# Performance work log

Hardware: AMD Instinct MI355X
Metric: run time of the kernel (lower is better)

The kernel has to match this reference:

```python
import jax, jax.numpy as jnp
import numpy as np


def setup_inputs() -> dict:
    key = jax.random.key(0)
    k1, k2 = jax.random.split(key)
    N, K, D = 32768, 1024, 512
    x = jax.random.normal(k1, (N, D), dtype=jnp.float32)
    centers = jax.random.normal(k2, (K, D), dtype=jnp.float32)
    return {"x": x, "centers": centers}


def reference(x, centers):
    # broadcasted (x[:,None]-c[None])**2 sum without the O(N*K*D) intermediate)
    x_sq = jnp.sum(x * x, axis=-1, keepdims=True)           # [N, 1]
    c_sq = jnp.sum(centers * centers, axis=-1)              # [K]
    cross = jnp.einsum('nd,kd->nk', x, centers)             # [N, K]
    norm_squared = x_sq + c_sq[None, :] - 2.0 * cross       # [N, K]
    # exp(-d/2) / sum_k exp(-d/2) == softmax(-d/2) over clusters
    probabilities = jax.nn.softmax(-0.5 * norm_squared, axis=1)
    return probabilities
```

## Files before the change

kernel.cpp:

```cpp
#include <hip/hip_runtime.h>
#include <stdint.h>


namespace {
constexpr int N_ROWS  = 32768;
constexpr int K_CL    = 1024;
constexpr int D_DIM   = 512;
constexpr int BM      = 64;
constexpr int THREADS = 512;
constexpr int WAVES   = 8;
constexpr int NSLICE  = 16;
}

typedef _Float16 f16_t;
typedef _Float16 f16x8 __attribute__((ext_vector_type(8)));
typedef _Float16 f16x4 __attribute__((ext_vector_type(4)));
typedef float    f32x16 __attribute__((ext_vector_type(16)));
typedef float    f32x4v __attribute__((ext_vector_type(4)));

__global__ __launch_bounds__(64) void prep_kernel(const float* __restrict__ centers,
                                                  f16_t* __restrict__ bpack,
                                                  float* __restrict__ bias) {
  const int col = blockIdx.x, lane = threadIdx.x;
  const int t  = lane >> 2;
  const int ks = (lane >> 1) & 1;
  const int kh = lane & 1;
  const float* src = centers + (size_t)col * D_DIM + lane * 8;
  f16x8 hi;
  float ssq = 0.f;
  #pragma unroll
  for (int i = 0; i < 8; ++i) {
    float v = src[i];
    ssq += v * v;
    hi[i] = (f16_t)v;
  }
  const int jh = col >> 9, cb = (col & 511) >> 5, c32 = col & 31;
  const size_t off = ((size_t)ks * 16 + cb) * 512 + (c32 * 2 + kh) * 8;
  *(f16x8*)(bpack + (size_t)(2 * t + jh) * 16384 + off) = hi;
  for (int o = 32; o; o >>= 1) ssq += __shfl_down(ssq, o, 64);
  if (lane == 0) bias[col] = -0.5f * ssq;
}

__global__ __launch_bounds__(THREADS, 2) void cluster_kernel(
    const float* __restrict__ x, const f16_t* __restrict__ bpack,
    const float* __restrict__ bias, float* __restrict__ out) {
  __shared__ __align__(16) char Ax[64 * 1024];
  __shared__ float red[WAVES * BM];
  __shared__ float fin[BM];

  const int tid  = threadIdx.x;
  const int wid  = tid >> 6;
  const int lane = tid & 63;
  const int l31  = lane & 31;
  const int h    = lane >> 5;
  const int brow = blockIdx.x * BM;

  const char* bbase = (const char*)bpack + wid * 2048 + (l31 * 2 + h) * 16;

#define LOADB8(S, DST)                                                         \
  {                                                                            \
    const char* p_ = bbase + (size_t)((S) & 31) * 32768;                       \
    (DST)[0] = *(const f16x8*)(p_);                       \
    (DST)[1] = *(const f16x8*)(p_ + 1024);                \
    (DST)[2] = *(const f16x8*)(p_ + 16384);               \
    (DST)[3] = *(const f16x8*)(p_ + 17408);               \
    (DST)[4] = *(const f16x8*)(p_ + 32768);               \
    (DST)[5] = *(const f16x8*)(p_ + 33792);               \
    (DST)[6] = *(const f16x8*)(p_ + 49152);               \
    (DST)[7] = *(const f16x8*)(p_ + 50176);               \
  }
#define COMPUTE16(B)                                                           \
  {                                                                            \
    _Pragma("unroll")                                                          \
    for (int j2_ = 0; j2_ < 2; ++j2_)                                          \
      _Pragma("unroll")                                                        \
      for (int ks_ = 0; ks_ < 2; ++ks_)                                        \
        _Pragma("unroll")                                                      \
        for (int c2_ = 0; c2_ < 2; ++c2_)                                      \
          _Pragma("unroll")                                                    \
          for (int rb_ = 0; rb_ < 2; ++rb_)                                    \
            acc[rb_][j2_ * 2 + c2_] = __builtin_amdgcn_mfma_f32_32x32x16_f16(  \
                a[rb_][ks_], (B)[j2_ * 4 + ks_ * 2 + c2_],                     \
                acc[rb_][j2_ * 2 + c2_], 0, 0, 0);                             \
  }

  f16x8 bA[8], bB[8];

  LOADB8(0, bA)

  {
    const float* xsrc = x + (size_t)brow * D_DIM;
    #pragma unroll
    for (int it = 0; it < 16; ++it) {
      const int idx = it * 512 + tid;
      const int r = idx >> 7, f = idx & 127;
      f32x4v v = __builtin_nontemporal_load(
          (const f32x4v*)(xsrc + (size_t)r * D_DIM + f * 4));
      f16x4 h4;
      h4[0] = (f16_t)v[0]; h4[1] = (f16_t)v[1];
      h4[2] = (f16_t)v[2]; h4[3] = (f16_t)v[3];
      *(f16x4*)(Ax + r * 1024 + ((f * 8) ^ ((r & 7) << 4))) = h4;
    }
  }
  __syncthreads();

  f32x16 acc[2][4];
  #pragma unroll
  for (int rb = 0; rb < 2; ++rb)
    #pragma unroll
    for (int cc = 0; cc < 4; ++cc)
      #pragma unroll
      for (int e = 0; e < 16; ++e) acc[rb][cc][e] = 0.f;

  const char* abase0 = Ax + l31 * 1024;
  const int swz = (l31 & 7) << 4;
  const int h16 = h * 16;
  f16x8 a[2][2];

  #pragma unroll
  for (int tt = 0; tt < 8; ++tt) {
    {
      const int T = 2 * tt;
      LOADB8(2 * (T + 1), bB)
      const int o0 = (T * 64 + h16) ^ swz;
      const int o1 = o0 ^ 32;
      a[0][0] = *(const f16x8*)(abase0 + o0);
      a[0][1] = *(const f16x8*)(abase0 + o1);
      a[1][0] = *(const f16x8*)(abase0 + 32768 + o0);
      a[1][1] = *(const f16x8*)(abase0 + 32768 + o1);
      COMPUTE16(bA)
    }
    {
      const int T = 2 * tt + 1;
      if (T < 15) LOADB8(2 * (T + 1), bA)
      const int o0 = (T * 64 + h16) ^ swz;
      const int o1 = o0 ^ 32;
      a[0][0] = *(const f16x8*)(abase0 + o0);
      a[0][1] = *(const f16x8*)(abase0 + o1);
      a[1][0] = *(const f16x8*)(abase0 + 32768 + o0);
      a[1][1] = *(const f16x8*)(abase0 + 32768 + o1);
      COMPUTE16(bB)
    }
  }

  float bcol[4];
  #pragma unroll
  for (int cc = 0; cc < 4; ++cc)
    bcol[cc] = bias[(cc >> 1) * 512 + wid * 64 + (cc & 1) * 32 + l31];

  float rr[2][16];
  #pragma unroll
  for (int rb = 0; rb < 2; ++rb)
    #pragma unroll
    for (int reg = 0; reg < 16; ++reg) {
      float m = -3.0e38f;
      #pragma unroll
      for (int cc = 0; cc < 4; ++cc) {
        float v = acc[rb][cc][reg] + bcol[cc];
        acc[rb][cc][reg] = v;
        m = fmaxf(m, v);
      }
      m = fmaxf(m, __shfl_xor(m, 1, 64));
      m = fmaxf(m, __shfl_xor(m, 2, 64));
      m = fmaxf(m, __shfl_xor(m, 4, 64));
      m = fmaxf(m, __shfl_xor(m, 8, 64));
      m = fmaxf(m, __shfl_xor(m, 16, 64));
      rr[rb][reg] = m;
    }
  __syncthreads();
  if (l31 == 0) {
    #pragma unroll
    for (int rb = 0; rb < 2; ++rb)
      #pragma unroll
      for (int reg = 0; reg < 16; ++reg)
        red[wid * BM + rb * 32 + (reg & 3) + 8 * (reg >> 2) + 4 * h] = rr[rb][reg];
  }
  __syncthreads();
  if (tid < BM) {
    float m = red[tid];
    #pragma unroll
    for (int w = 1; w < WAVES; ++w) m = fmaxf(m, red[w * BM + tid]);
    fin[tid] = m;
  }
  __syncthreads();

  #pragma unroll
  for (int rb = 0; rb < 2; ++rb)
    #pragma unroll
    for (int reg = 0; reg < 16; ++reg) {
      const float m = fin[rb * 32 + (reg & 3) + 8 * (reg >> 2) + 4 * h];
      float s = 0.f;
      #pragma unroll
      for (int cc = 0; cc < 4; ++cc) {
        float e = __expf(acc[rb][cc][reg] - m);
        acc[rb][cc][reg] = e;
        s += e;
      }
      s += __shfl_xor(s, 1, 64);
      s += __shfl_xor(s, 2, 64);
      s += __shfl_xor(s, 4, 64);
      s += __shfl_xor(s, 8, 64);
      s += __shfl_xor(s, 16, 64);
      rr[rb][reg] = s;
    }
  __syncthreads();
  if (l31 == 0) {
    #pragma unroll
    for (int rb = 0; rb < 2; ++rb)
      #pragma unroll
      for (int reg = 0; reg < 16; ++reg)
        red[wid * BM + rb * 32 + (reg & 3) + 8 * (reg >> 2) + 4 * h] = rr[rb][reg];
  }
  __syncthreads();
  if (tid < BM) {
    float s = 0.f;
    #pragma unroll
    for (int w = 0; w < WAVES; ++w) s += red[w * BM + tid];
    fin[tid] = 1.0f / s;
  }
  __syncthreads();

  #pragma unroll
  for (int rb = 0; rb < 2; ++rb)
    #pragma unroll
    for (int reg = 0; reg < 16; ++reg) {
      const int row = rb * 32 + (reg & 3) + 8 * (reg >> 2) + 4 * h;
      const float rs = fin[row];
      #pragma unroll
      for (int cc = 0; cc < 4; ++cc) {
        const int col = (cc >> 1) * 512 + wid * 64 + (cc & 1) * 32 + l31;
        out[(size_t)(brow + row) * K_CL + col] = acc[rb][cc][reg] * rs;
      }
    }
}

extern "C" void kernel_launch(void* const* d_in, const int* in_sizes, int n_in,
                              void* d_out, int out_size, void* d_ws, size_t ws_size,
                              hipStream_t stream) {
  const float* x       = (const float*)d_in[0];
  const float* centers = (const float*)d_in[1];
  float* out = (float*)d_out;

  f16_t* bpack = (f16_t*)d_ws;
  float* bias  = (float*)((char*)d_ws + (size_t)32 * 32768);

  prep_kernel<<<K_CL, 64, 0, stream>>>(centers, bpack, bias);
  cluster_kernel<<<N_ROWS / BM, THREADS, 0, stream>>>(x, bpack, bias, out);
}
```

Before: 93.93 us.

## Split GEMM and softmax into separate kernels with int16 intermediate in output buffer

The fused kernel is split in two. The GEMM kernel writes the cross term as fixed-point int16, scaled by 128, into the first half of each output row. A separate row-wise softmax kernel then reads it back, adds the bias and writes fp32 probabilities in place. This removes the block-level LDS reductions and barriers from the GEMM epilogue. The cost is extra global memory traffic and a quantisation error of about 1/128 in the logits.

```diff
diff --git a/kernel.cpp b/kernel.cpp
--- a/kernel.cpp
+++ b/kernel.cpp
@@ -9,12 +9,12 @@
 constexpr int BM      = 64;
 constexpr int THREADS = 512;
 constexpr int WAVES   = 8;
-constexpr int NSLICE  = 16;
 }
 
 typedef _Float16 f16_t;
 typedef _Float16 f16x8 __attribute__((ext_vector_type(8)));
 typedef _Float16 f16x4 __attribute__((ext_vector_type(4)));
+typedef short    s16x8 __attribute__((ext_vector_type(8)));
 typedef float    f32x16 __attribute__((ext_vector_type(16)));
 typedef float    f32x4v __attribute__((ext_vector_type(4)));
 
@@ -41,12 +41,10 @@
   if (lane == 0) bias[col] = -0.5f * ssq;
 }
 
-__global__ __launch_bounds__(THREADS, 2) void cluster_kernel(
+__global__ __launch_bounds__(THREADS, 2) void gemm_kernel(
     const float* __restrict__ x, const f16_t* __restrict__ bpack,
-    const float* __restrict__ bias, float* __restrict__ out) {
+    float* __restrict__ out) {
   __shared__ __align__(16) char Ax[64 * 1024];
-  __shared__ float red[WAVES * BM];
-  __shared__ float fin[BM];
 
   const int tid  = threadIdx.x;
   const int wid  = tid >> 6;
@@ -143,95 +141,75 @@
     }
   }
 
-  float bcol[4];
-  #pragma unroll
-  for (int cc = 0; cc < 4; ++cc)
-    bcol[cc] = bias[(cc >> 1) * 512 + wid * 64 + (cc & 1) * 32 + l31];
-
-  float rr[2][16];
-  #pragma unroll
-  for (int rb = 0; rb < 2; ++rb)
-    #pragma unroll
-    for (int reg = 0; reg < 16; ++reg) {
-      float m = -3.0e38f;
-      #pragma unroll
-      for (int cc = 0; cc < 4; ++cc) {
-        float v = acc[rb][cc][reg] + bcol[cc];
-        acc[rb][cc][reg] = v;
-        m = fmaxf(m, v);
-      }
-      m = fmaxf(m, __shfl_xor(m, 1, 64));
-      m = fmaxf(m, __shfl_xor(m, 2, 64));
-      m = fmaxf(m, __shfl_xor(m, 4, 64));
-      m = fmaxf(m, __shfl_xor(m, 8, 64));
-      m = fmaxf(m, __shfl_xor(m, 16, 64));
-      rr[rb][reg] = m;
-    }
-  __syncthreads();
-  if (l31 == 0) {
-    #pragma unroll
-    for (int rb = 0; rb < 2; ++rb)
-      #pragma unroll
-      for (int reg = 0; reg < 16; ++reg)
-        red[wid * BM + rb * 32 + (reg & 3) + 8 * (reg >> 2) + 4 * h] = rr[rb][reg];
-  }
-  __syncthreads();
-  if (tid < BM) {
-    float m = red[tid];
-    #pragma unroll
-    for (int w = 1; w < WAVES; ++w) m = fmaxf(m, red[w * BM + tid]);
-    fin[tid] = m;
-  }
-  __syncthreads();
-
-  #pragma unroll
-  for (int rb = 0; rb < 2; ++rb)
-    #pragma unroll
-    for (int reg = 0; reg < 16; ++reg) {
-      const float m = fin[rb * 32 + (reg & 3) + 8 * (reg >> 2) + 4 * h];
-      float s = 0.f;
-      #pragma unroll
-      for (int cc = 0; cc < 4; ++cc) {
-        float e = __expf(acc[rb][cc][reg] - m);
-        acc[rb][cc][reg] = e;
-        s += e;
-      }
-      s += __shfl_xor(s, 1, 64);
-      s += __shfl_xor(s, 2, 64);
-      s += __shfl_xor(s, 4, 64);
-      s += __shfl_xor(s, 8, 64);
-      s += __shfl_xor(s, 16, 64);
-      rr[rb][reg] = s;
-    }
-  __syncthreads();
-  if (l31 == 0) {
-    #pragma unroll
-    for (int rb = 0; rb < 2; ++rb)
-      #pragma unroll
-      for (int reg = 0; reg < 16; ++reg)
-        red[wid * BM + rb * 32 + (reg & 3) + 8 * (reg >> 2) + 4 * h] = rr[rb][reg];
-  }
-  __syncthreads();
-  if (tid < BM) {
-    float s = 0.f;
-    #pragma unroll
-    for (int w = 0; w < WAVES; ++w) s += red[w * BM + tid];
-    fin[tid] = 1.0f / s;
-  }
-  __syncthreads();
-
   #pragma unroll
   for (int rb = 0; rb < 2; ++rb)
     #pragma unroll
     for (int reg = 0; reg < 16; ++reg) {
       const int row = rb * 32 + (reg & 3) + 8 * (reg >> 2) + 4 * h;
-      const float rs = fin[row];
+      short* lp = (short*)(out + (size_t)(brow + row) * K_CL);
       #pragma unroll
       for (int cc = 0; cc < 4; ++cc) {
         const int col = (cc >> 1) * 512 + wid * 64 + (cc & 1) * 32 + l31;
-        out[(size_t)(brow + row) * K_CL + col] = acc[rb][cc][reg] * rs;
+        float v = acc[rb][cc][reg] * 128.f;
+        v = fminf(fmaxf(v, -32000.f), 32000.f);
+        lp[col] = (short)__float2int_rn(v);
       }
     }
+}
+
+__global__ __launch_bounds__(256) void softmax_kernel(
+    const float* __restrict__ bias, float* __restrict__ out) {
+  const int tid  = threadIdx.x;
+  const int row  = blockIdx.x * 4 + (tid >> 6);
+  const int lane = tid & 63;
+
+  float* rp = out + (size_t)row * K_CL;
+  const short* lp = (const short*)rp + lane * 16;
+  s16x8 q0 = *(const s16x8*)(lp);
+  s16x8 q1 = *(const s16x8*)(lp + 8);
+
+  const float* bp = bias + lane * 16;
+  float v[16];
+  #pragma unroll
+  for (int i = 0; i < 8; ++i) {
+    v[i]     = (float)q0[i] * (1.f / 128.f) + bp[i];
+    v[i + 8] = (float)q1[i] * (1.f / 128.f) + bp[i + 8];
+  }
+
+  float m = v[0];
+  #pragma unroll
+  for (int i = 1; i < 16; ++i) m = fmaxf(m, v[i]);
+  m = fmaxf(m, __shfl_xor(m, 1, 64));
+  m = fmaxf(m, __shfl_xor(m, 2, 64));
+  m = fmaxf(m, __shfl_xor(m, 4, 64));
+  m = fmaxf(m, __shfl_xor(m, 8, 64));
+  m = fmaxf(m, __shfl_xor(m, 16, 64));
+  m = fmaxf(m, __shfl_xor(m, 32, 64));
+
+  float s = 0.f;
+  #pragma unroll
+  for (int i = 0; i < 16; ++i) {
+    v[i] = __expf(v[i] - m);
+    s += v[i];
+  }
+  s += __shfl_xor(s, 1, 64);
+  s += __shfl_xor(s, 2, 64);
+  s += __shfl_xor(s, 4, 64);
+  s += __shfl_xor(s, 8, 64);
+  s += __shfl_xor(s, 16, 64);
+  s += __shfl_xor(s, 32, 64);
+  const float rinv = 1.f / s;
+
+  float* wp = rp + lane * 16;
+  #pragma unroll
+  for (int j = 0; j < 4; ++j) {
+    f32x4v w;
+    w[0] = v[j * 4 + 0] * rinv;
+    w[1] = v[j * 4 + 1] * rinv;
+    w[2] = v[j * 4 + 2] * rinv;
+    w[3] = v[j * 4 + 3] * rinv;
+    __builtin_nontemporal_store(w, (f32x4v*)(wp + j * 4));
+  }
 }
 
 extern "C" void kernel_launch(void* const* d_in, const int* in_sizes, int n_in,
@@ -245,5 +223,6 @@
   float* bias  = (float*)((char*)d_ws + (size_t)32 * 32768);
 
   prep_kernel<<<K_CL, 64, 0, stream>>>(centers, bpack, bias);
-  cluster_kernel<<<N_ROWS / BM, THREADS, 0, stream>>>(x, bpack, bias, out);
-}
+  gemm_kernel<<<N_ROWS / BM, THREADS, 0, stream>>>(x, bpack, out);
+  softmax_kernel<<<N_ROWS / 4, 256, 0, stream>>>(bias, out);
+}
```

Result: slower. 166.7 us (+77.4%).
